# Optimization experiments

Measured on AMD Instinct MI355X. Metric: run time of the kernel, lower is better.

Reference implementation:

```python
import jax, jax.numpy as jnp
import numpy as np

B, C, H, W, K = 2, 3, 256, 256, 51  # output H,W; filter size K; input is (H+K-1, W+K-1)


def _sepconv(inp, vertical, horizontal):
    # inp: [B,C,H+K-1,W+K-1]; vertical/horizontal: [B,K,H,W]
    Kf = vertical.shape[1]
    Ho, Wo = vertical.shape[2], vertical.shape[3]
    rows = jnp.stack([inp[:, :, i:i + Ho, :] for i in range(Kf)], axis=0)

    def body(acc, j):
        # window for horizontal offset j: [K,B,C,Ho,Wo]
        win = jax.lax.dynamic_slice_in_dim(rows, j, Wo, axis=4)
        # contract over vertical taps i with per-pixel vertical kernel
        vcon = jnp.einsum('kbchw,bkhw->bchw', win, vertical)
        # weight by per-pixel horizontal tap j and accumulate
        acc = acc + vcon * horizontal[:, j][:, None, :, :]
        return acc, None

    acc0 = jnp.zeros((inp.shape[0], inp.shape[1], Ho, Wo), inp.dtype)
    out, _ = jax.lax.scan(body, acc0, jnp.arange(Kf))
    return out


def setup_inputs() -> dict:
    key = jax.random.key(0)
    k1, k2, k3 = jax.random.split(key, 3)
    tenInput = jax.random.normal(k1, (B, C, H + K - 1, W + K - 1), dtype=jnp.float32)
    tenVertical = jax.random.normal(k2, (B, K, H, W), dtype=jnp.float32)
    tenHorizontal = jax.random.normal(k3, (B, K, H, W), dtype=jnp.float32)
    return {"tenInput": tenInput, "tenVertical": tenVertical, "tenHorizontal": tenHorizontal}


def reference(tenInput, tenVertical, tenHorizontal):
    return _sepconv(tenInput, tenVertical, tenHorizontal)
```

## Files before the change

### kernel.cpp

```cpp
#include <hip/hip_runtime.h>


namespace {
constexpr int KK = 51;
constexpr int NB = 2;
constexpr int NC = 3;
constexpr int HH = 256;
constexpr int WW = 256;
constexpr int IN_H = HH + KK - 1;
constexpr int IN_W = WW + KK - 1;

constexpr int TILE_W = 64;
constexpr int TILE_H = 8;
constexpr int NTX = 8;
constexpr int R = 8;
constexpr int NTY = 8;
constexpr int NS = 4;
constexpr int NTHREADS = NTX * NTY * NS;
constexpr int HALO_W = TILE_W + KK - 1;
constexpr int LDS_W = 116;
constexpr int LDS_H = TILE_H + KK - 1;
constexpr int KSTRIDE = HH * WW;
constexpr int HCH = 4 * TILE_H * TILE_W;
}

__device__ __forceinline__ float fget(const float4 v, int i) {
  return (i == 0) ? v.x : (i == 1) ? v.y : (i == 2) ? v.z : v.w;
}

template <int P, int JJ>
__device__ __forceinline__ void fma_jtap(const float4 (&v4)[4][2], const float4 (&w4)[4][3],
                                         const float4 ha, const float4 hb, float (&acc)[R]) {
#pragma unroll
  for (int rx = 0; rx < R; ++rx) {
    const int k  = rx + JJ;
    const int sl = (P + k / 4) % 3;
    const int cp = k & 3;
    const int vh = rx >> 2, vc = rx & 3;
    float tv = fget(v4[0][vh], vc) * fget(w4[0][sl], cp);
    tv = fmaf(fget(v4[1][vh], vc), fget(w4[1][sl], cp), tv);
    tv = fmaf(fget(v4[2][vh], vc), fget(w4[2][sl], cp), tv);
    tv = fmaf(fget(v4[3][vh], vc), fget(w4[3][sl], cp), tv);
    const float hv = (rx < 4) ? fget(ha, vc) : fget(hb, vc);
    acc[rx] = fmaf(hv, tv, acc[rx]);
  }
}

template <int P>
__device__ __forceinline__ void full_chunk(const float4 (&v4)[4][2], float4 (&w4)[4][3],
                                           const int (&woff)[4], int wcol,
                                           const float* hb, int off0, int off1,
                                           float (&acc)[R], const float* smem) {
  const float4 h0a = *reinterpret_cast<const float4*>(hb + off0);
  const float4 h0b = *reinterpret_cast<const float4*>(hb + off1);
  const float4 h1a = *reinterpret_cast<const float4*>(hb + 512 + off0);
  const float4 h1b = *reinterpret_cast<const float4*>(hb + 512 + off1);
  fma_jtap<P, 0>(v4, w4, h0a, h0b, acc);
  const float4 h2a = *reinterpret_cast<const float4*>(hb + 1024 + off0);
  const float4 h2b = *reinterpret_cast<const float4*>(hb + 1024 + off1);
  fma_jtap<P, 1>(v4, w4, h1a, h1b, acc);
  const float4 h3a = *reinterpret_cast<const float4*>(hb + 1536 + off0);
  const float4 h3b = *reinterpret_cast<const float4*>(hb + 1536 + off1);
  fma_jtap<P, 2>(v4, w4, h2a, h2b, acc);
  fma_jtap<P, 3>(v4, w4, h3a, h3b, acc);
#pragma unroll
  for (int ib = 0; ib < 4; ++ib)
    w4[ib][P] = *reinterpret_cast<const float4*>(&smem[woff[ib] + wcol]);
}

__global__ __launch_bounds__(NTHREADS, 1)
void sepconv_kernel(
    const float* __restrict__ inp,
    const float* __restrict__ vert,
    const float* __restrict__ horiz,
    float* __restrict__ out)
{
  __shared__ float lds[LDS_H * LDS_W];
  __shared__ float hbuf[2 * HCH];

  const int tid = threadIdx.x;
  const int tx  = tid & (NTX - 1);
  const int ty  = (tid >> 3) & (NTY - 1);
  const int s   = tid >> 6;

  const int x0 = blockIdx.x * TILE_W;
  const int y0 = blockIdx.y * TILE_H;
  const int bc = blockIdx.z;
  const int b  = bc / NC;
  const int c  = bc % NC;

  {
    const float* src = inp + (((size_t)(b * NC + c)) * IN_H + y0) * IN_W + x0;
    constexpr int total2 = LDS_H * (HALO_W / 2);
    for (int e = tid; e < total2; e += NTHREADS) {
      const int col2 = e % (HALO_W / 2);
      const int r    = e / (HALO_W / 2);
      const float2 v = *reinterpret_cast<const float2*>(src + (size_t)r * IN_W + col2 * 2);
      float* dst = &lds[r * LDS_W + col2 * 2];
      dst[0] = v.x; dst[1] = v.y;
    }
  }

  const float* hblk = horiz + (((size_t)b * KK) * HH + y0) * WW + x0;
  int jj_[2], goff_[2], ldso_[2];
#pragma unroll
  for (int r = 0; r < 2; ++r) {
    const int p   = r * 256 + tid;
    const int jj  = p >> 7;
    const int rem = p & 127;
    const int row = rem >> 4;
    const int c4  = rem & 15;
    const int q   = (c4 - row) & 15;
    jj_[r]   = jj;
    goff_[r] = row * WW + q * 4;
    ldso_[r] = (r * 256 + (tid & ~63)) * 4;
  }
  auto stage = [&](int cc, int bufn) {
#pragma unroll
    for (int r = 0; r < 2; ++r) {
      const int j  = 4 * cc + jj_[r];
      const int jc = (j <= 50) ? j : 50;
      const float* g = hblk + (size_t)jc * KSTRIDE + goff_[r];
      float* l = &hbuf[bufn * HCH + ldso_[r]];
      __builtin_amdgcn_global_load_lds((const __attribute__((address_space(1))) void*)g,
                                       (__attribute__((address_space(3))) void*)l, 16, 0, 0);
    }
  };

  stage(0, 0);
  __syncthreads();

  const int lx = tx * R;
  const int xg = x0 + lx;
  const int yg = y0 + ty;

  const int off0 = ty * 64 + ((2 * tx + ty) & 15) * 4;
  const int off1 = ty * 64 + ((2 * tx + 1 + ty) & 15) * 4;

  float acc[R];
#pragma unroll
  for (int rx = 0; rx < R; ++rx) acc[rx] = 0.f;

  const int blk0 = (s == 0) ? 0 : (3 * s + 1);
  const int nblk = (s == 0) ? 4 : 3;

  const float* vbase = vert + (((size_t)b * KK) * HH + yg) * WW + xg;

  int ccn = 1, buf = 0;

#pragma unroll 1
  for (int t = 0; t < 4; ++t) {
    const bool act = (t < nblk);
    float4 v4[4][2];
    float4 w4[4][3];
    int    woff[4];
    if (act) {
      const int ibase = (blk0 + t) * 4;
#pragma unroll
      for (int ib = 0; ib < 4; ++ib) {
        const int iv = ibase + ib;
        const int ic = (iv <= 50) ? iv : 50;
        float4 va = *reinterpret_cast<const float4*>(vbase + (size_t)ic * KSTRIDE);
        float4 vb = *reinterpret_cast<const float4*>(vbase + (size_t)ic * KSTRIDE + 4);
        if (iv > 50) { va = make_float4(0.f, 0.f, 0.f, 0.f); vb = va; }
        v4[ib][0] = va; v4[ib][1] = vb;
        woff[ib] = (ty + ic) * LDS_W;
        const float4* p = reinterpret_cast<const float4*>(&lds[woff[ib] + lx]);
        w4[ib][0] = p[0]; w4[ib][1] = p[1]; w4[ib][2] = p[2];
      }
    }

#pragma unroll 1
    for (int g = 0; g < 4; ++g) {
      const int base = lx + 12 * g + 12;
      stage(ccn, buf ^ 1); ccn = (ccn == 12) ? 0 : ccn + 1;
      if (act) full_chunk<0>(v4, w4, woff, base + 0, hbuf + buf * HCH, off0, off1, acc, lds);
      __syncthreads(); buf ^= 1;
      stage(ccn, buf ^ 1); ccn = (ccn == 12) ? 0 : ccn + 1;
      if (act) full_chunk<1>(v4, w4, woff, base + 4, hbuf + buf * HCH, off0, off1, acc, lds);
      __syncthreads(); buf ^= 1;
      stage(ccn, buf ^ 1); ccn = (ccn == 12) ? 0 : ccn + 1;
      if (act) full_chunk<2>(v4, w4, woff, base + 8, hbuf + buf * HCH, off0, off1, acc, lds);
      __syncthreads(); buf ^= 1;
    }

    stage(ccn, buf ^ 1); ccn = (ccn == 12) ? 0 : ccn + 1;
    if (act) {
      const float* hb = hbuf + buf * HCH;
      const float4 e0a = *reinterpret_cast<const float4*>(hb + off0);
      const float4 e0b = *reinterpret_cast<const float4*>(hb + off1);
      const float4 e1a = *reinterpret_cast<const float4*>(hb + 512 + off0);
      const float4 e1b = *reinterpret_cast<const float4*>(hb + 512 + off1);
      const float4 e2a = *reinterpret_cast<const float4*>(hb + 1024 + off0);
      const float4 e2b = *reinterpret_cast<const float4*>(hb + 1024 + off1);
      fma_jtap<0, 0>(v4, w4, e0a, e0b, acc);
      fma_jtap<0, 1>(v4, w4, e1a, e1b, acc);
      fma_jtap<0, 2>(v4, w4, e2a, e2b, acc);
    }
    __syncthreads(); buf ^= 1;
  }

  if (s > 0) {
    float* p = &lds[((s - 1) * 64 + ty * NTX + tx) * R];
#pragma unroll
    for (int rx = 0; rx < R; ++rx) p[rx] = acc[rx];
  }
  __syncthreads();
  if (s == 0) {
#pragma unroll
    for (int g = 0; g < 3; ++g) {
      const float* p = &lds[(g * 64 + ty * NTX + tx) * R];
#pragma unroll
      for (int rx = 0; rx < R; ++rx) acc[rx] += p[rx];
    }
    float* o = out + (((size_t)(b * NC + c)) * HH + yg) * WW + xg;
    *reinterpret_cast<float4*>(o)     = make_float4(acc[0], acc[1], acc[2], acc[3]);
    *reinterpret_cast<float4*>(o + 4) = make_float4(acc[4], acc[5], acc[6], acc[7]);
  }
}

extern "C" void kernel_launch(void* const* d_in, const int* in_sizes, int n_in,
                              void* d_out, int out_size, void* d_ws, size_t ws_size,
                              hipStream_t stream) {
  const float* inp   = (const float*)d_in[0];
  const float* vert  = (const float*)d_in[1];
  const float* horiz = (const float*)d_in[2];
  float* out = (float*)d_out;

  dim3 grid(WW / TILE_W, HH / TILE_H, NB * NC);
  sepconv_kernel<<<grid, NTHREADS, 0, stream>>>(inp, vert, horiz, out);
}
```

Measured before the change: 143.2 us.

## Triple-buffer horizontal-tap staging with partial vmcnt waits and one barrier per step

Replaces the double-buffered horizontal-weight staging with a three-buffer ring that keeps two async global-to-LDS loads in flight. Each step waits only until the oldest outstanding load has landed (vmcnt(2)), then issues a raw barrier and the next stage. The goal is to hide global load latency behind compute instead of draining all loads at every __syncthreads. It costs an extra LDS buffer and relies on the vmcnt counting matching the exact number of outstanding loads per thread. The v4 global loads inside the loop also count toward vmcnt, which could break that assumption.

```diff
diff --git a/kernel.cpp b/kernel.cpp
--- a/kernel.cpp
+++ b/kernel.cpp
@@ -22,6 +22,7 @@
 constexpr int LDS_H = TILE_H + KK - 1;
 constexpr int KSTRIDE = HH * WW;
 constexpr int HCH = 4 * TILE_H * TILE_W;
+constexpr int NSTEPS = 52;
 }
 
 __device__ __forceinline__ float fget(const float4 v, int i) {
@@ -76,7 +77,7 @@
     float* __restrict__ out)
 {
   __shared__ float lds[LDS_H * LDS_W];
-  __shared__ float hbuf[2 * HCH];
+  __shared__ float hbuf[3 * HCH];
 
   const int tid = threadIdx.x;
   const int tx  = tid & (NTX - 1);
@@ -128,6 +129,7 @@
   };
 
   stage(0, 0);
+  stage(1, 1);
   __syncthreads();
 
   const int lx = tx * R;
@@ -146,7 +148,21 @@
 
   const float* vbase = vert + (((size_t)b * KK) * HH + yg) * WW + xg;
 
-  int ccn = 1, buf = 0;
+  int nstep = 0, bcur = 0, ccn = 2;
+
+  auto syncstage = [&]() {
+    if (nstep == NSTEPS - 1) {
+      asm volatile("s_waitcnt vmcnt(0)" ::: "memory");
+    } else {
+      asm volatile("s_waitcnt vmcnt(2)" ::: "memory");
+    }
+    __builtin_amdgcn_s_barrier();
+    if (nstep + 2 < NSTEPS) {
+      stage(ccn, (bcur + 2) % 3);
+      ccn = (ccn == 12) ? 0 : ccn + 1;
+    }
+  };
+  auto adv = [&]() { bcur = (bcur + 1) % 3; ++nstep; };
 
 #pragma unroll 1
   for (int t = 0; t < 4; ++t) {
@@ -173,20 +189,20 @@
 #pragma unroll 1
     for (int g = 0; g < 4; ++g) {
       const int base = lx + 12 * g + 12;
-      stage(ccn, buf ^ 1); ccn = (ccn == 12) ? 0 : ccn + 1;
-      if (act) full_chunk<0>(v4, w4, woff, base + 0, hbuf + buf * HCH, off0, off1, acc, lds);
-      __syncthreads(); buf ^= 1;
-      stage(ccn, buf ^ 1); ccn = (ccn == 12) ? 0 : ccn + 1;
-      if (act) full_chunk<1>(v4, w4, woff, base + 4, hbuf + buf * HCH, off0, off1, acc, lds);
-      __syncthreads(); buf ^= 1;
-      stage(ccn, buf ^ 1); ccn = (ccn == 12) ? 0 : ccn + 1;
-      if (act) full_chunk<2>(v4, w4, woff, base + 8, hbuf + buf * HCH, off0, off1, acc, lds);
-      __syncthreads(); buf ^= 1;
-    }
-
-    stage(ccn, buf ^ 1); ccn = (ccn == 12) ? 0 : ccn + 1;
+      syncstage();
+      if (act) full_chunk<0>(v4, w4, woff, base + 0, hbuf + bcur * HCH, off0, off1, acc, lds);
+      adv();
+      syncstage();
+      if (act) full_chunk<1>(v4, w4, woff, base + 4, hbuf + bcur * HCH, off0, off1, acc, lds);
+      adv();
+      syncstage();
+      if (act) full_chunk<2>(v4, w4, woff, base + 8, hbuf + bcur * HCH, off0, off1, acc, lds);
+      adv();
+    }
+
+    syncstage();
     if (act) {
-      const float* hb = hbuf + buf * HCH;
+      const float* hb = hbuf + bcur * HCH;
       const float4 e0a = *reinterpret_cast<const float4*>(hb + off0);
       const float4 e0b = *reinterpret_cast<const float4*>(hb + off1);
       const float4 e1a = *reinterpret_cast<const float4*>(hb + 512 + off0);
@@ -197,9 +213,10 @@
       fma_jtap<0, 1>(v4, w4, e1a, e1b, acc);
       fma_jtap<0, 2>(v4, w4, e2a, e2b, acc);
     }
-    __syncthreads(); buf ^= 1;
-  }
-
+    adv();
+  }
+
+  __syncthreads();
   if (s > 0) {
     float* p = &lds[((s - 1) * 64 + ty * NTX + tx) * R];
 #pragma unroll
```

After: 143.1 us. Within noise of the previous version (-0.1%).

## Load half of horizontal taps directly into registers, halve LDS staging

Applied to the files above, without the earlier changes.

Horizontal taps 2 and 3 of each group of four are now loaded straight from global memory into registers one chunk ahead, and only taps 0 and 1 are staged through LDS with async global-to-LDS copies. The horizontal LDS buffer is halved and each thread issues one staging load per chunk instead of two. This cuts LDS traffic and staging work, but adds per-thread global loads that are exposed to latency and raises register pressure.

```diff
diff --git a/kernel.cpp b/kernel.cpp
--- a/kernel.cpp
+++ b/kernel.cpp
@@ -21,7 +21,7 @@
 constexpr int LDS_W = 116;
 constexpr int LDS_H = TILE_H + KK - 1;
 constexpr int KSTRIDE = HH * WW;
-constexpr int HCH = 4 * TILE_H * TILE_W;
+constexpr int HCH = 2 * TILE_H * TILE_W;
 }
 
 __device__ __forceinline__ float fget(const float4 v, int i) {
@@ -50,19 +50,21 @@
 __device__ __forceinline__ void full_chunk(const float4 (&v4)[4][2], float4 (&w4)[4][3],
                                            const int (&woff)[4], int wcol,
                                            const float* hb, int off0, int off1,
+                                           float4 (&hr)[4], int j2n, int j3n,
+                                           const float* hbase,
                                            float (&acc)[R], const float* smem) {
+  fma_jtap<P, 2>(v4, w4, hr[0], hr[1], acc);
+  fma_jtap<P, 3>(v4, w4, hr[2], hr[3], acc);
+  hr[0] = *reinterpret_cast<const float4*>(hbase + (size_t)j2n * KSTRIDE);
+  hr[1] = *reinterpret_cast<const float4*>(hbase + (size_t)j2n * KSTRIDE + 4);
+  hr[2] = *reinterpret_cast<const float4*>(hbase + (size_t)j3n * KSTRIDE);
+  hr[3] = *reinterpret_cast<const float4*>(hbase + (size_t)j3n * KSTRIDE + 4);
   const float4 h0a = *reinterpret_cast<const float4*>(hb + off0);
   const float4 h0b = *reinterpret_cast<const float4*>(hb + off1);
   const float4 h1a = *reinterpret_cast<const float4*>(hb + 512 + off0);
   const float4 h1b = *reinterpret_cast<const float4*>(hb + 512 + off1);
   fma_jtap<P, 0>(v4, w4, h0a, h0b, acc);
-  const float4 h2a = *reinterpret_cast<const float4*>(hb + 1024 + off0);
-  const float4 h2b = *reinterpret_cast<const float4*>(hb + 1024 + off1);
   fma_jtap<P, 1>(v4, w4, h1a, h1b, acc);
-  const float4 h3a = *reinterpret_cast<const float4*>(hb + 1536 + off0);
-  const float4 h3b = *reinterpret_cast<const float4*>(hb + 1536 + off1);
-  fma_jtap<P, 2>(v4, w4, h2a, h2b, acc);
-  fma_jtap<P, 3>(v4, w4, h3a, h3b, acc);
 #pragma unroll
   for (int ib = 0; ib < 4; ++ib)
     w4[ib][P] = *reinterpret_cast<const float4*>(&smem[woff[ib] + wcol]);
@@ -102,37 +104,34 @@
   }
 
   const float* hblk = horiz + (((size_t)b * KK) * HH + y0) * WW + x0;
-  int jj_[2], goff_[2], ldso_[2];
-#pragma unroll
-  for (int r = 0; r < 2; ++r) {
-    const int p   = r * 256 + tid;
-    const int jj  = p >> 7;
-    const int rem = p & 127;
-    const int row = rem >> 4;
-    const int c4  = rem & 15;
-    const int q   = (c4 - row) & 15;
-    jj_[r]   = jj;
-    goff_[r] = row * WW + q * 4;
-    ldso_[r] = (r * 256 + (tid & ~63)) * 4;
-  }
+  const int jj_  = tid >> 7;
+  const int rem  = tid & 127;
+  const int hrow = rem >> 4;
+  const int c4_  = rem & 15;
+  const int q_   = (c4_ - hrow) & 15;
+  const int goff = hrow * WW + q_ * 4;
+  const int ldso = (tid & ~63) * 4;
   auto stage = [&](int cc, int bufn) {
-#pragma unroll
-    for (int r = 0; r < 2; ++r) {
-      const int j  = 4 * cc + jj_[r];
-      const int jc = (j <= 50) ? j : 50;
-      const float* g = hblk + (size_t)jc * KSTRIDE + goff_[r];
-      float* l = &hbuf[bufn * HCH + ldso_[r]];
-      __builtin_amdgcn_global_load_lds((const __attribute__((address_space(1))) void*)g,
-                                       (__attribute__((address_space(3))) void*)l, 16, 0, 0);
-    }
+    const int j = 4 * cc + jj_;
+    const float* g = hblk + (size_t)j * KSTRIDE + goff;
+    float* l = &hbuf[bufn * HCH + ldso];
+    __builtin_amdgcn_global_load_lds((const __attribute__((address_space(1))) void*)g,
+                                     (__attribute__((address_space(3))) void*)l, 16, 0, 0);
   };
-
-  stage(0, 0);
-  __syncthreads();
 
   const int lx = tx * R;
   const int xg = x0 + lx;
   const int yg = y0 + ty;
+  const float* hbase = horiz + (((size_t)b * KK) * HH + yg) * WW + xg;
+
+  stage(0, 0);
+  float4 hr[4];
+  hr[0] = *reinterpret_cast<const float4*>(hbase + (size_t)2 * KSTRIDE);
+  hr[1] = *reinterpret_cast<const float4*>(hbase + (size_t)2 * KSTRIDE + 4);
+  hr[2] = *reinterpret_cast<const float4*>(hbase + (size_t)3 * KSTRIDE);
+  hr[3] = *reinterpret_cast<const float4*>(hbase + (size_t)3 * KSTRIDE + 4);
+  __syncthreads();
+  int buf = 0;
 
   const int off0 = ty * 64 + ((2 * tx + ty) & 15) * 4;
   const int off1 = ty * 64 + ((2 * tx + 1 + ty) & 15) * 4;
@@ -145,8 +144,6 @@
   const int nblk = (s == 0) ? 4 : 3;
 
   const float* vbase = vert + (((size_t)b * KK) * HH + yg) * WW + xg;
-
-  int ccn = 1, buf = 0;
 
 #pragma unroll 1
   for (int t = 0; t < 4; ++t) {
@@ -173,29 +170,40 @@
 #pragma unroll 1
     for (int g = 0; g < 4; ++g) {
       const int base = lx + 12 * g + 12;
-      stage(ccn, buf ^ 1); ccn = (ccn == 12) ? 0 : ccn + 1;
-      if (act) full_chunk<0>(v4, w4, woff, base + 0, hbuf + buf * HCH, off0, off1, acc, lds);
+      const int cc = 3 * g;
+      stage(cc + 1, buf ^ 1);
+      if (act) full_chunk<0>(v4, w4, woff, base + 0, hbuf + buf * HCH, off0, off1,
+                             hr, 4 * (cc + 1) + 2, 4 * (cc + 1) + 3, hbase, acc, lds);
       __syncthreads(); buf ^= 1;
-      stage(ccn, buf ^ 1); ccn = (ccn == 12) ? 0 : ccn + 1;
-      if (act) full_chunk<1>(v4, w4, woff, base + 4, hbuf + buf * HCH, off0, off1, acc, lds);
+      stage(cc + 2, buf ^ 1);
+      if (act) full_chunk<1>(v4, w4, woff, base + 4, hbuf + buf * HCH, off0, off1,
+                             hr, 4 * (cc + 2) + 2, 4 * (cc + 2) + 3, hbase, acc, lds);
       __syncthreads(); buf ^= 1;
-      stage(ccn, buf ^ 1); ccn = (ccn == 12) ? 0 : ccn + 1;
-      if (act) full_chunk<2>(v4, w4, woff, base + 8, hbuf + buf * HCH, off0, off1, acc, lds);
+      stage(cc + 3, buf ^ 1);
+      {
+        const int ccn = cc + 3;
+        const int j2n = 4 * ccn + 2;
+        const int j3n = (4 * ccn + 3 <= 50) ? 4 * ccn + 3 : 50;
+        if (act) full_chunk<2>(v4, w4, woff, base + 8, hbuf + buf * HCH, off0, off1,
+                               hr, j2n, j3n, hbase, acc, lds);
+      }
       __syncthreads(); buf ^= 1;
     }
 
-    stage(ccn, buf ^ 1); ccn = (ccn == 12) ? 0 : ccn + 1;
+    stage(0, buf ^ 1);
     if (act) {
+      fma_jtap<0, 2>(v4, w4, hr[0], hr[1], acc);
+      hr[0] = *reinterpret_cast<const float4*>(hbase + (size_t)2 * KSTRIDE);
+      hr[1] = *reinterpret_cast<const float4*>(hbase + (size_t)2 * KSTRIDE + 4);
+      hr[2] = *reinterpret_cast<const float4*>(hbase + (size_t)3 * KSTRIDE);
+      hr[3] = *reinterpret_cast<const float4*>(hbase + (size_t)3 * KSTRIDE + 4);
       const float* hb = hbuf + buf * HCH;
       const float4 e0a = *reinterpret_cast<const float4*>(hb + off0);
       const float4 e0b = *reinterpret_cast<const float4*>(hb + off1);
       const float4 e1a = *reinterpret_cast<const float4*>(hb + 512 + off0);
       const float4 e1b = *reinterpret_cast<const float4*>(hb + 512 + off1);
-      const float4 e2a = *reinterpret_cast<const float4*>(hb + 1024 + off0);
-      const float4 e2b = *reinterpret_cast<const float4*>(hb + 1024 + off1);
       fma_jtap<0, 0>(v4, w4, e0a, e0b, acc);
       fma_jtap<0, 1>(v4, w4, e1a, e1b, acc);
-      fma_jtap<0, 2>(v4, w4, e2a, e2b, acc);
     }
     __syncthreads(); buf ^= 1;
   }
```

Result: slower. 169.0 us (+18.0%).

## Split vertical taps across two grid halves and sum partials in second kernel

Applied to the files above, without the earlier changes.

Doubles the grid by splitting the 51 vertical taps into two halves (rows 0-25 and 26-50), each block computing a partial output into a workspace buffer, then a small kernel adds the two halves into the output. This shrinks the per-block input LDS tile and the per-warpgroup tap work, raising block count to fill more CUs on a small grid. The cost is a second launch, extra global traffic for the partials, and horizontal weights are still streamed in full by both halves.

```diff
diff --git a/kernel.cpp b/kernel.cpp
--- a/kernel.cpp
+++ b/kernel.cpp
@@ -19,9 +19,10 @@
 constexpr int NTHREADS = NTX * NTY * NS;
 constexpr int HALO_W = TILE_W + KK - 1;
 constexpr int LDS_W = 116;
-constexpr int LDS_H = TILE_H + KK - 1;
+constexpr int LDS_H = 33;
 constexpr int KSTRIDE = HH * WW;
 constexpr int HCH = 4 * TILE_H * TILE_W;
+constexpr int OUTN = NB * NC * HH * WW;
 }
 
 __device__ __forceinline__ float fget(const float4 v, int i) {
@@ -73,7 +74,7 @@
     const float* __restrict__ inp,
     const float* __restrict__ vert,
     const float* __restrict__ horiz,
-    float* __restrict__ out)
+    float* __restrict__ ws)
 {
   __shared__ float lds[LDS_H * LDS_W];
   __shared__ float hbuf[2 * HCH];
@@ -85,17 +86,23 @@
 
   const int x0 = blockIdx.x * TILE_W;
   const int y0 = blockIdx.y * TILE_H;
-  const int bc = blockIdx.z;
+  const int zz = blockIdx.z;
+  const int bc = zz % (NB * NC);
+  const int half = zz / (NB * NC);
   const int b  = bc / NC;
   const int c  = bc % NC;
 
+  const int ROWBASE = half * 26;
+  const int ROWMAX  = half ? 50 : 25;
+
   {
-    const float* src = inp + (((size_t)(b * NC + c)) * IN_H + y0) * IN_W + x0;
+    const float* src = inp + (((size_t)(b * NC + c)) * IN_H) * IN_W + x0;
     constexpr int total2 = LDS_H * (HALO_W / 2);
     for (int e = tid; e < total2; e += NTHREADS) {
       const int col2 = e % (HALO_W / 2);
       const int r    = e / (HALO_W / 2);
-      const float2 v = *reinterpret_cast<const float2*>(src + (size_t)r * IN_W + col2 * 2);
+      const int gr   = min(y0 + ROWBASE + r, IN_H - 1);
+      const float2 v = *reinterpret_cast<const float2*>(src + (size_t)gr * IN_W + col2 * 2);
       float* dst = &lds[r * LDS_W + col2 * 2];
       dst[0] = v.x; dst[1] = v.y;
     }
@@ -106,12 +113,11 @@
 #pragma unroll
   for (int r = 0; r < 2; ++r) {
     const int p   = r * 256 + tid;
-    const int jj  = p >> 7;
     const int rem = p & 127;
     const int row = rem >> 4;
     const int c4  = rem & 15;
     const int q   = (c4 - row) & 15;
-    jj_[r]   = jj;
+    jj_[r]   = p >> 7;
     goff_[r] = row * WW + q * 4;
     ldso_[r] = (r * 256 + (tid & ~63)) * 4;
   }
@@ -129,6 +135,7 @@
 
   stage(0, 0);
   __syncthreads();
+  int buf = 0, ccn = 1;
 
   const int lx = tx * R;
   const int xg = x0 + lx;
@@ -141,30 +148,28 @@
 #pragma unroll
   for (int rx = 0; rx < R; ++rx) acc[rx] = 0.f;
 
-  const int blk0 = (s == 0) ? 0 : (3 * s + 1);
-  const int nblk = (s == 0) ? 4 : 3;
+  const int blk0 = (s < 3) ? 2 * s : 6;
+  const int nblk = (s < 3) ? 2 : 1;
 
   const float* vbase = vert + (((size_t)b * KK) * HH + yg) * WW + xg;
 
-  int ccn = 1, buf = 0;
-
 #pragma unroll 1
-  for (int t = 0; t < 4; ++t) {
+  for (int t = 0; t < 2; ++t) {
     const bool act = (t < nblk);
     float4 v4[4][2];
     float4 w4[4][3];
     int    woff[4];
     if (act) {
-      const int ibase = (blk0 + t) * 4;
+      const int ibase = ROWBASE + (blk0 + t) * 4;
 #pragma unroll
       for (int ib = 0; ib < 4; ++ib) {
         const int iv = ibase + ib;
-        const int ic = (iv <= 50) ? iv : 50;
+        const int ic = (iv <= ROWMAX) ? iv : ROWMAX;
         float4 va = *reinterpret_cast<const float4*>(vbase + (size_t)ic * KSTRIDE);
         float4 vb = *reinterpret_cast<const float4*>(vbase + (size_t)ic * KSTRIDE + 4);
-        if (iv > 50) { va = make_float4(0.f, 0.f, 0.f, 0.f); vb = va; }
+        if (iv > ROWMAX) { va = make_float4(0.f, 0.f, 0.f, 0.f); vb = va; }
         v4[ib][0] = va; v4[ib][1] = vb;
-        woff[ib] = (ty + ic) * LDS_W;
+        woff[ib] = (ty + ic - ROWBASE) * LDS_W;
         const float4* p = reinterpret_cast<const float4*>(&lds[woff[ib] + lx]);
         w4[ib][0] = p[0]; w4[ib][1] = p[1]; w4[ib][2] = p[2];
       }
@@ -213,10 +218,19 @@
 #pragma unroll
       for (int rx = 0; rx < R; ++rx) acc[rx] += p[rx];
     }
-    float* o = out + (((size_t)(b * NC + c)) * HH + yg) * WW + xg;
+    float* o = ws + (size_t)half * OUTN + (((size_t)(b * NC + c)) * HH + yg) * WW + xg;
     *reinterpret_cast<float4*>(o)     = make_float4(acc[0], acc[1], acc[2], acc[3]);
     *reinterpret_cast<float4*>(o + 4) = make_float4(acc[4], acc[5], acc[6], acc[7]);
   }
+}
+
+__global__ __launch_bounds__(256)
+void sum_halves(const float4* __restrict__ a, const float4* __restrict__ b,
+                float4* __restrict__ o)
+{
+  const int i = blockIdx.x * 256 + threadIdx.x;
+  const float4 x = a[i], y = b[i];
+  o[i] = make_float4(x.x + y.x, x.y + y.y, x.z + y.z, x.w + y.w);
 }
 
 extern "C" void kernel_launch(void* const* d_in, const int* in_sizes, int n_in,
@@ -226,7 +240,12 @@
   const float* vert  = (const float*)d_in[1];
   const float* horiz = (const float*)d_in[2];
   float* out = (float*)d_out;
-
-  dim3 grid(WW / TILE_W, HH / TILE_H, NB * NC);
-  sepconv_kernel<<<grid, NTHREADS, 0, stream>>>(inp, vert, horiz, out);
-}
+  float* ws  = (float*)d_ws;
+
+  dim3 grid(WW / TILE_W, HH / TILE_H, 2 * NB * NC);
+  sepconv_kernel<<<grid, NTHREADS, 0, stream>>>(inp, vert, horiz, ws);
+
+  const int n4 = OUTN / 4;
+  sum_halves<<<n4 / 256, 256, 0, stream>>>(
+      (const float4*)ws, (const float4*)(ws + OUTN), (float4*)out);
+}
```

Result: no change. 144.4 us (+0.8%).
